# Optimization experiments

Hardware: AMD Instinct MI355X
Metric: run time of the kernel (lower is better)

## Reference

```python
import jax, jax.numpy as jnp
import numpy as np
import math

D_MODEL = 2048
N_HEADS = 16
HEAD_DIM = D_MODEL // N_HEADS  # 128
SEQ = 2048
BATCH = 1


def make_freqs(seq_len, head_dim, theta=10000.0):
    # standard rotary frequencies: freqs_cis = exp(i * t * inv_freq)
    inv_freq = 1.0 / (theta ** (np.arange(0, head_dim, 2, dtype=np.float32) / head_dim))
    t = np.arange(seq_len, dtype=np.float32)
    ang = np.outer(t, inv_freq)  # [seq, head_dim/2]
    return jnp.asarray(np.cos(ang)), jnp.asarray(np.sin(ang))


def setup_inputs() -> dict:
    key = jax.random.key(0)
    ks = jax.random.split(key, 6)
    x = jax.random.normal(ks[0], (BATCH, SEQ, D_MODEL), dtype=jnp.float32)
    freqs_cos, freqs_sin = make_freqs(SEQ, HEAD_DIM)
    # causal additive mask, broadcastable to [b, h, s, s]
    mask = jnp.where(jnp.tril(jnp.ones((SEQ, SEQ), dtype=bool)), 0.0, -1e9).astype(jnp.float32)[None, None]
    scale = 0.02
    wq = jax.random.normal(ks[1], (D_MODEL, D_MODEL), dtype=jnp.float32) * scale
    wk = jax.random.normal(ks[2], (D_MODEL, D_MODEL), dtype=jnp.float32) * scale
    wv = jax.random.normal(ks[3], (D_MODEL, D_MODEL), dtype=jnp.float32) * scale
    wo = jax.random.normal(ks[4], (D_MODEL, D_MODEL), dtype=jnp.float32) * scale
    return {"x": x, "freqs_cos": freqs_cos, "freqs_sin": freqs_sin, "mask": mask,
            "wq": wq, "wk": wk, "wv": wv, "wo": wo}


def _apply_rotary(q, k, cos, sin):
    # q, k: [b, s, h, hd]; cos/sin: [s, hd/2]
    def rot(t):
        tr = t.reshape(*t.shape[:-1], -1, 2)  # [b, s, h, hd/2, 2]
        re, im = tr[..., 0], tr[..., 1]
        c = cos[None, :, None, :]
        s = sin[None, :, None, :]
        # complex multiply (re + i im) * (c + i s)
        out_re = re * c - im * s
        out_im = re * s + im * c
        return jnp.stack([out_re, out_im], axis=-1).reshape(t.shape)
    return rot(q), rot(k)


def reference(x, freqs_cos, freqs_sin, mask, wq, wk, wv, wo):
    b, s, _ = x.shape
    # QKV projections (nn.Linear with no bias: x @ W^T; W is square so use x @ W
    # with W stored already-transposed -- weights here are random so x @ W is faithful math)
    q = (x @ wq).reshape(b, s, N_HEADS, HEAD_DIM)
    k = (x @ wk).reshape(b, s, N_HEADS, HEAD_DIM)
    v = (x @ wv).reshape(b, s, N_HEADS, HEAD_DIM)
    q, k = _apply_rotary(q, k, freqs_cos, freqs_sin)
    # [b, h, s_q, s_k]
    scores = jnp.einsum("bqhd,bkhd->bhqk", q, k) / math.sqrt(HEAD_DIM)
    scores = scores + mask
    probs = jax.nn.softmax(scores.astype(jnp.float32), axis=-1).astype(q.dtype)
    out = jnp.einsum("bhqk,bkhd->bqhd", probs, v).reshape(b, s, N_HEADS * HEAD_DIM)
    return out @ wo
```

## Files before the change

### kernel.cpp

```cpp
#include <hip/hip_runtime.h>
#include <hip/hip_bf16.h>
#include <math.h>

#define SEQ 2048
#define DM 2048
#define NH 16
#define HD 128
#define QKV_N 6144

typedef __bf16 bf16;
typedef __bf16 bf16x8 __attribute__((ext_vector_type(8)));
typedef __bf16 bf16x4v __attribute__((ext_vector_type(4)));
typedef __bf16 bf16x2v __attribute__((ext_vector_type(2)));
typedef float f32x4 __attribute__((ext_vector_type(4)));

__device__ inline int sw_idx64(int row, int chunk) {
    return (row * 8 + (chunk ^ (row & 7))) * 8;
}
__device__ inline int sw_idx128(int row, int chunk) {
    return (row * 16 + (chunk ^ (row & 15))) * 8;
}

__device__ inline void async16(const void* g, void* l) {
    __builtin_amdgcn_global_load_lds((const __attribute__((address_space(1))) void*)g,
                                     (__attribute__((address_space(3))) void*)l, 16, 0, 0);
}

__global__ __launch_bounds__(256) void k_prep(const float* __restrict__ wq,
                                              const float* __restrict__ wk,
                                              const float* __restrict__ wv,
                                              const float* __restrict__ wo,
                                              bf16* __restrict__ wT, bf16* __restrict__ woT,
                                              const float* __restrict__ x,
                                              bf16* __restrict__ xb) {
    const int z = blockIdx.z;
    const int t = threadIdx.x;
    if (z == 4) {
        int bid = blockIdx.y * 32 + blockIdx.x;
#pragma unroll
        for (int j = 0; j < 4; ++j) {
            int i = bid * 1024 + j * 256 + t;
            float4 v = ((const float4*)x)[i];
            bf16x4v o;
            o.x = (bf16)v.x; o.y = (bf16)v.y; o.z = (bf16)v.z; o.w = (bf16)v.w;
            ((bf16x4v*)xb)[i] = o;
        }
        return;
    }
    __shared__ bf16 tile[64][66];
    const float* src = (z == 0) ? wq : (z == 1) ? wk : (z == 2) ? wv : wo;
    bf16* dst = (z < 3) ? (wT + (size_t)z * DM * DM) : woT;
    const int bx = blockIdx.x * 64, by = blockIdx.y * 64;
#pragma unroll
    for (int j = 0; j < 4; ++j) {
        int idx = j * 256 + t;
        int r = idx >> 4, cg = idx & 15;
        float4 v = *(const float4*)&src[(size_t)(by + r) * DM + bx + cg * 4];
        bf16x4v o;
        o.x = (bf16)v.x; o.y = (bf16)v.y; o.z = (bf16)v.z; o.w = (bf16)v.w;
        *(bf16x4v*)&tile[r][cg * 4] = o;
    }
    __syncthreads();
#pragma unroll
    for (int j = 0; j < 4; ++j) {
        int idx = j * 256 + t;
        int r = idx >> 4, cg = idx & 15;
        bf16x4v o;
        o.x = tile[cg * 4 + 0][r];
        o.y = tile[cg * 4 + 1][r];
        o.z = tile[cg * 4 + 2][r];
        o.w = tile[cg * 4 + 3][r];
        *(bf16x4v*)&dst[(size_t)(bx + r) * DM + by + cg * 4] = o;
    }
}

__global__ __launch_bounds__(256) void k_rope_vt(bf16* __restrict__ qkv,
                                                 const float* __restrict__ cosT,
                                                 const float* __restrict__ sinT,
                                                 bf16* __restrict__ vT) {
    const int t = threadIdx.x;
    if (blockIdx.x >= 1024) {
        int g = (blockIdx.x - 1024) * 256 + t;
        int s = g >> 8;
        int cg = g & 255;
        int h = cg >> 4, w8 = cg & 15;
        size_t base = (size_t)s * QKV_N + DM + h * HD + w8 * 8;
        float4 cv = *(const float4*)&cosT[s * 64 + w8 * 4];
        float4 sv = *(const float4*)&sinT[s * 64 + w8 * 4];
        float cc[4] = {cv.x, cv.y, cv.z, cv.w};
        float ss[4] = {sv.x, sv.y, sv.z, sv.w};
        bf16x8 k = *(bf16x8*)&qkv[base];
        bf16x8 o;
#pragma unroll
        for (int p = 0; p < 4; ++p) {
            float re = (float)k[2 * p], im = (float)k[2 * p + 1];
            o[2 * p]     = (bf16)(re * cc[p] - im * ss[p]);
            o[2 * p + 1] = (bf16)(re * ss[p] + im * cc[p]);
        }
        *(bf16x8*)&qkv[base] = o;
        return;
    }
    __shared__ bf16 tile[64][66];
    const int bx = (blockIdx.x & 31) * 64, by = (blockIdx.x >> 5) * 64;
#pragma unroll
    for (int j = 0; j < 4; ++j) {
        int idx = j * 256 + t;
        int r = idx >> 4, cg = idx & 15;
        *(bf16x4v*)&tile[r][cg * 4] =
            *(const bf16x4v*)&qkv[(size_t)(by + r) * QKV_N + 2 * DM + bx + cg * 4];
    }
    __syncthreads();
#pragma unroll
    for (int j = 0; j < 4; ++j) {
        int idx = j * 256 + t;
        int r = idx >> 4, cg = idx & 15;
        bf16x4v o;
        o.x = tile[cg * 4 + 0][r];
        o.y = tile[cg * 4 + 1][r];
        o.z = tile[cg * 4 + 2][r];
        o.w = tile[cg * 4 + 3][r];
        *(bf16x4v*)&vT[(size_t)(bx + r) * SEQ + by + cg * 4] = o;
    }
}

template <typename OutT, int BN>
__device__ __forceinline__ void gemm_body(const bf16* __restrict__ A,
                                          const bf16* __restrict__ Bt,
                                          OutT* __restrict__ C,
                                          int N, int K, size_t bm, size_t bn,
                                          bf16* As, bf16* Bs) {
    constexpr int NI = BN / 32;
    const int t = threadIdx.x;
    const int lane = t & 63;
    const int w = t >> 6;
    const int wr = (w >> 1) * 64, wc = (w & 1) * (BN / 2);
    const int l15 = lane & 15, quad = lane >> 4;
    f32x4 acc[4][NI];
#pragma unroll
    for (int i = 0; i < 4; ++i)
#pragma unroll
        for (int j = 0; j < NI; ++j) acc[i][j] = (f32x4){0.f, 0.f, 0.f, 0.f};

    for (int kt = 0; kt < K; kt += 64) {
#pragma unroll
        for (int j = 0; j < 4; ++j) {
            int c = j * 256 + t;
            int row = c >> 3, g = ((c & 7) ^ (row & 7)) * 8;
            async16(&A[(bm + row) * K + kt + g], &As[c * 8]);
        }
#pragma unroll
        for (int j = 0; j < NI; ++j) {
            int c = j * 256 + t;
            int row = c >> 3, g = ((c & 7) ^ (row & 7)) * 8;
            async16(&Bt[(bn + row) * K + kt + g], &Bs[c * 8]);
        }
        __syncthreads();
#pragma unroll
        for (int kh = 0; kh < 2; ++kh) {
            bf16x8 af[4], bfm[NI];
#pragma unroll
            for (int mi = 0; mi < 4; ++mi)
                af[mi] = *(const bf16x8*)&As[sw_idx64(wr + mi * 16 + l15, kh * 4 + quad)];
#pragma unroll
            for (int ni = 0; ni < NI; ++ni)
                bfm[ni] = *(const bf16x8*)&Bs[sw_idx64(wc + ni * 16 + l15, kh * 4 + quad)];
#pragma unroll
            for (int mi = 0; mi < 4; ++mi)
#pragma unroll
                for (int ni = 0; ni < NI; ++ni)
                    acc[mi][ni] = __builtin_amdgcn_mfma_f32_16x16x32_bf16(
                        af[mi], bfm[ni], acc[mi][ni], 0, 0, 0);
        }
        __syncthreads();
    }
#pragma unroll
    for (int mi = 0; mi < 4; ++mi)
#pragma unroll
        for (int ni = 0; ni < NI; ++ni)
#pragma unroll
            for (int r = 0; r < 4; ++r) {
                size_t row = bm + wr + mi * 16 + quad * 4 + r;
                size_t col = bn + wc + ni * 16 + l15;
                C[row * (size_t)N + col] = (OutT)acc[mi][ni][r];
            }
}

template <typename OutT, int BN>
__global__ __launch_bounds__(256) void k_gemm_bt(const bf16* __restrict__ A,
                                                 const bf16* __restrict__ Bt,
                                                 OutT* __restrict__ C,
                                                 int M, int N, int K) {
    __shared__ bf16 As[128 * 64];
    __shared__ bf16 Bs[BN * 64];
    size_t bm = (size_t)blockIdx.y * 128, bn = (size_t)blockIdx.x * BN;
    gemm_body<OutT, BN>(A, Bt, C, N, K, bm, bn, As, Bs);
}

__global__ __launch_bounds__(256) void k_flash(const bf16* __restrict__ qkv,
                                               const bf16* __restrict__ vT,
                                               const float* __restrict__ cosT,
                                               const float* __restrict__ sinT,
                                               bf16* __restrict__ out) {
    __shared__ bf16 Ks[2][64 * 128];
    __shared__ bf16 Vs[2][128 * 64];
    __shared__ bf16 Pl[4][16 * 64];
    const int t = threadIdx.x;
    const int lane = t & 63;
    const int w = t >> 6;
    const int l15 = lane & 15, quad = lane >> 4;
    const int b = blockIdx.x;
    const int h = (b & 7) * 2 + ((b >> 3) & 1);
    const int qb = (b < 256) ? (31 - (b >> 4)) : ((b >> 4) - 16);
    const int q0w = qb * 64 + w * 16;
    const float sc2 = 0.08838834764831845f * 1.4426950408889634f;

    const size_t qrow = (size_t)(q0w + l15) * QKV_N + h * HD;
    bf16x8 aq[4];
#pragma unroll
    for (int u = 0; u < 4; ++u)
        aq[u] = *(const bf16x8*)&qkv[qrow + u * 32 + quad * 8];
#pragma unroll
    for (int u = 0; u < 4; ++u) {
        float4 cv = *(const float4*)&cosT[(q0w + l15) * 64 + u * 16 + quad * 4];
        float4 sv = *(const float4*)&sinT[(q0w + l15) * 64 + u * 16 + quad * 4];
        float cc[4] = {cv.x, cv.y, cv.z, cv.w};
        float ss[4] = {sv.x, sv.y, sv.z, sv.w};
        bf16x8 q = aq[u], rq;
#pragma unroll
        for (int p = 0; p < 4; ++p) {
            float re = (float)q[2 * p], im = (float)q[2 * p + 1];
            rq[2 * p]     = (bf16)(re * cc[p] - im * ss[p]);
            rq[2 * p + 1] = (bf16)(re * ss[p] + im * cc[p]);
        }
        aq[u] = rq;
    }

    f32x4 o[8];
#pragma unroll
    for (int c = 0; c < 8; ++c) o[c] = (f32x4){0.f, 0.f, 0.f, 0.f};
    float l_r[4] = {0.f, 0.f, 0.f, 0.f};

    int krow[4], kg[4], vrow[4], vg[4];
#pragma unroll
    for (int j = 0; j < 4; ++j) {
        int c = j * 256 + t;
        krow[j] = c >> 4; kg[j] = ((c & 15) ^ (krow[j] & 15)) * 8;
        vrow[j] = c >> 3; vg[j] = ((c & 7) ^ (vrow[j] & 7)) * 8;
    }
    auto stage = [&](int buf, int kt2) {
        const int kb2 = kt2 * 64;
#pragma unroll
        for (int j = 0; j < 4; ++j)
            async16(&qkv[(size_t)(kb2 + krow[j]) * QKV_N + DM + h * HD + kg[j]],
                    &Ks[buf][(j * 256 + t) * 8]);
#pragma unroll
        for (int j = 0; j < 4; ++j)
            async16(&vT[(size_t)(h * HD + vrow[j]) * SEQ + kb2 + vg[j]],
                    &Vs[buf][(j * 256 + t) * 8]);
    };

    const int n64 = qb + 1;
    stage(0, 0);
    for (int kt = 0; kt < n64; ++kt) {
        const int cb = kt & 1;
        const int kbase = kt * 64;
        const bool pre = (kt + 1 < n64);
        if (pre) {
            stage(cb ^ 1, kt + 1);
            asm volatile("s_waitcnt vmcnt(12)" ::: "memory");
        } else {
            asm volatile("s_waitcnt vmcnt(4)" ::: "memory");
        }
        __builtin_amdgcn_s_barrier();
        asm volatile("" ::: "memory");

        f32x4 s4[4];
        __builtin_amdgcn_s_setprio(1);
#pragma unroll
        for (int sub = 0; sub < 4; ++sub) {
            f32x4 z = (f32x4){0.f, 0.f, 0.f, 0.f};
#pragma unroll
            for (int u = 0; u < 4; ++u) {
                bf16x8 kv = *(const bf16x8*)&Ks[cb][sw_idx128(sub * 16 + l15, u * 4 + quad)];
                z = __builtin_amdgcn_mfma_f32_16x16x32_bf16(aq[u], kv, z, 0, 0, 0);
            }
            s4[sub] = z;
        }
        __builtin_amdgcn_s_setprio(0);
        const bool masked = (kt == n64 - 1);
#pragma unroll
        for (int sub = 0; sub < 4; ++sub)
#pragma unroll
            for (int r = 0; r < 4; ++r) {
                float p = __builtin_amdgcn_exp2f(s4[sub][r] * sc2);
                if (masked)
                    p = (kbase + sub * 16 + l15 <= q0w + quad * 4 + r) ? p : 0.f;
                l_r[r] += p;
                int rowp = quad * 4 + r;
                int col = sub * 16 + l15;
                Pl[w][(rowp * 8 + ((col >> 3) ^ (rowp & 7))) * 8 + (col & 7)] = (bf16)p;
            }
        if (pre) asm volatile("s_waitcnt vmcnt(8)" ::: "memory");
        else     asm volatile("s_waitcnt vmcnt(0)" ::: "memory");
        __builtin_amdgcn_s_barrier();
        __asm__ __volatile__("s_waitcnt lgkmcnt(0)" ::: "memory");
        bf16x8 pf[2];
#pragma unroll
        for (int kk = 0; kk < 2; ++kk)
            pf[kk] = *(const bf16x8*)&Pl[w][sw_idx64(l15, kk * 4 + quad)];
        __builtin_amdgcn_s_setprio(1);
#pragma unroll
        for (int c = 0; c < 8; ++c)
#pragma unroll
            for (int kk = 0; kk < 2; ++kk) {
                bf16x8 vb = *(const bf16x8*)&Vs[cb][sw_idx64(c * 16 + l15, kk * 4 + quad)];
                o[c] = __builtin_amdgcn_mfma_f32_16x16x32_bf16(pf[kk], vb, o[c], 0, 0, 0);
            }
        __builtin_amdgcn_s_setprio(0);
        asm volatile("" ::: "memory");
        __builtin_amdgcn_s_barrier();
        asm volatile("" ::: "memory");
    }

    float rl[4];
#pragma unroll
    for (int r = 0; r < 4; ++r) {
        float l = l_r[r];
        l += __shfl_xor(l, 1, 16);
        l += __shfl_xor(l, 2, 16);
        l += __shfl_xor(l, 4, 16);
        l += __shfl_xor(l, 8, 16);
        rl[r] = 1.0f / l;
    }
#pragma unroll
    for (int c = 0; c < 8; ++c)
#pragma unroll
        for (int r = 0; r < 4; ++r)
            out[(size_t)(q0w + quad * 4 + r) * DM + h * HD + c * 16 + l15] =
                (bf16)(o[c][r] * rl[r]);
}

extern "C" void kernel_launch(void* const* d_in, const int* in_sizes, int n_in,
                              void* d_out, int out_size, void* d_ws, size_t ws_size,
                              hipStream_t stream) {
    const float* x  = (const float*)d_in[0];
    const float* fc = (const float*)d_in[1];
    const float* fs = (const float*)d_in[2];
    const float* wq = (const float*)d_in[4];
    const float* wk = (const float*)d_in[5];
    const float* wv = (const float*)d_in[6];
    const float* wo = (const float*)d_in[7];
    float* out = (float*)d_out;

    char* ws = (char*)d_ws;
    bf16* xb  = (bf16*)(ws);
    bf16* wT  = (bf16*)(ws + (size_t)(8u  << 20));
    bf16* woT = (bf16*)(ws + (size_t)(32u << 20));
    bf16* qkv = (bf16*)(ws + (size_t)(40u << 20));
    bf16* vT  = (bf16*)(ws + (size_t)(64u << 20));

    k_prep<<<dim3(32, 32, 5), 256, 0, stream>>>(wq, wk, wv, wo, wT, woT, x, xb);
    k_gemm_bt<bf16, 128><<<dim3(48, 16), 256, 0, stream>>>(xb, wT, qkv, SEQ, QKV_N, DM);
    k_rope_vt<<<3072, 256, 0, stream>>>(qkv, fc, fs, vT);
    k_flash<<<512, 256, 0, stream>>>(qkv, vT, fc, fs, xb);
    k_gemm_bt<float, 64><<<dim3(32, 16), 256, 0, stream>>>(xb, woT, out, SEQ, DM, DM);
}
```

Measured before the change: 285.5 us.

## Pair high and low causal query blocks in one 512-thread flash block sharing K/V

The flash attention kernel now runs 256 blocks of 512 threads. Each block pairs a long causal query block (31-p) with a short one (p) for the same head, and both 4-wave groups share the same staged K/V tiles. This halves global K/V traffic for the short block's tiles and balances work per block. The cost is that the low-block waves sit idle at barriers once they pass their last tile, while the block keeps looping for the high block. Larger blocks may also reduce occupancy.

```diff
diff --git a/kernel.cpp b/kernel.cpp
--- a/kernel.cpp
+++ b/kernel.cpp
@@ -196,22 +196,27 @@
     gemm_body<OutT, BN>(A, Bt, C, N, K, bm, bn, As, Bs);
 }
 
-__global__ __launch_bounds__(256) void k_flash(const bf16* __restrict__ qkv,
+__global__ __launch_bounds__(512) void k_flash(const bf16* __restrict__ qkv,
                                                const bf16* __restrict__ vT,
                                                const float* __restrict__ cosT,
                                                const float* __restrict__ sinT,
                                                bf16* __restrict__ out) {
     __shared__ bf16 Ks[2][64 * 128];
     __shared__ bf16 Vs[2][128 * 64];
-    __shared__ bf16 Pl[4][16 * 64];
+    __shared__ bf16 Pl[8][16 * 64];
     const int t = threadIdx.x;
     const int lane = t & 63;
     const int w = t >> 6;
+    const int wl = w & 3;
+    const int g = w >> 2;
     const int l15 = lane & 15, quad = lane >> 4;
     const int b = blockIdx.x;
-    const int h = (b & 7) * 2 + ((b >> 3) & 1);
-    const int qb = (b < 256) ? (31 - (b >> 4)) : ((b >> 4) - 16);
-    const int q0w = qb * 64 + w * 16;
+    const int hc = b & 15;
+    const int h = (hc & 7) * 2 + (hc >> 3);
+    const int p = b >> 4;
+    const int qbH = 31 - p, qbL = p;
+    const int myQb = g ? qbL : qbH;
+    const int q0w = myQb * 64 + wl * 16;
     const float sc2 = 0.08838834764831845f * 1.4426950408889634f;
 
     const size_t qrow = (size_t)(q0w + l15) * QKV_N + h * HD;
@@ -227,10 +232,10 @@
         float ss[4] = {sv.x, sv.y, sv.z, sv.w};
         bf16x8 q = aq[u], rq;
 #pragma unroll
-        for (int p = 0; p < 4; ++p) {
-            float re = (float)q[2 * p], im = (float)q[2 * p + 1];
-            rq[2 * p]     = (bf16)(re * cc[p] - im * ss[p]);
-            rq[2 * p + 1] = (bf16)(re * ss[p] + im * cc[p]);
+        for (int pp = 0; pp < 4; ++pp) {
+            float re = (float)q[2 * pp], im = (float)q[2 * pp + 1];
+            rq[2 * pp]     = (bf16)(re * cc[pp] - im * ss[pp]);
+            rq[2 * pp + 1] = (bf16)(re * ss[pp] + im * cc[pp]);
         }
         aq[u] = rq;
     }
@@ -240,83 +245,88 @@
     for (int c = 0; c < 8; ++c) o[c] = (f32x4){0.f, 0.f, 0.f, 0.f};
     float l_r[4] = {0.f, 0.f, 0.f, 0.f};
 
-    int krow[4], kg[4], vrow[4], vg[4];
-#pragma unroll
-    for (int j = 0; j < 4; ++j) {
-        int c = j * 256 + t;
-        krow[j] = c >> 4; kg[j] = ((c & 15) ^ (krow[j] & 15)) * 8;
-        vrow[j] = c >> 3; vg[j] = ((c & 7) ^ (vrow[j] & 7)) * 8;
+    int krow[2], kg[2], vrow[2], vg[2];
+#pragma unroll
+    for (int j = 0; j < 2; ++j) {
+        int c2 = j * 512 + t;
+        krow[j] = c2 >> 4; kg[j] = ((c2 & 15) ^ (krow[j] & 15)) * 8;
+        vrow[j] = c2 >> 3; vg[j] = ((c2 & 7) ^ (vrow[j] & 7)) * 8;
     }
     auto stage = [&](int buf, int kt2) {
         const int kb2 = kt2 * 64;
 #pragma unroll
-        for (int j = 0; j < 4; ++j)
+        for (int j = 0; j < 2; ++j)
             async16(&qkv[(size_t)(kb2 + krow[j]) * QKV_N + DM + h * HD + kg[j]],
-                    &Ks[buf][(j * 256 + t) * 8]);
-#pragma unroll
-        for (int j = 0; j < 4; ++j)
+                    &Ks[buf][(j * 512 + t) * 8]);
+#pragma unroll
+        for (int j = 0; j < 2; ++j)
             async16(&vT[(size_t)(h * HD + vrow[j]) * SEQ + kb2 + vg[j]],
-                    &Vs[buf][(j * 256 + t) * 8]);
+                    &Vs[buf][(j * 512 + t) * 8]);
     };
 
-    const int n64 = qb + 1;
+    const int nT = qbH + 1;
     stage(0, 0);
-    for (int kt = 0; kt < n64; ++kt) {
+    for (int kt = 0; kt < nT; ++kt) {
         const int cb = kt & 1;
         const int kbase = kt * 64;
-        const bool pre = (kt + 1 < n64);
+        const bool pre = (kt + 1 < nT);
         if (pre) {
             stage(cb ^ 1, kt + 1);
-            asm volatile("s_waitcnt vmcnt(12)" ::: "memory");
+            asm volatile("s_waitcnt vmcnt(6)" ::: "memory");
         } else {
-            asm volatile("s_waitcnt vmcnt(4)" ::: "memory");
+            asm volatile("s_waitcnt vmcnt(2)" ::: "memory");
         }
         __builtin_amdgcn_s_barrier();
         asm volatile("" ::: "memory");
 
-        f32x4 s4[4];
-        __builtin_amdgcn_s_setprio(1);
-#pragma unroll
-        for (int sub = 0; sub < 4; ++sub) {
-            f32x4 z = (f32x4){0.f, 0.f, 0.f, 0.f};
-#pragma unroll
-            for (int u = 0; u < 4; ++u) {
-                bf16x8 kv = *(const bf16x8*)&Ks[cb][sw_idx128(sub * 16 + l15, u * 4 + quad)];
-                z = __builtin_amdgcn_mfma_f32_16x16x32_bf16(aq[u], kv, z, 0, 0, 0);
+        const bool active = (kt <= myQb);
+        if (active) {
+            f32x4 s4[4];
+            __builtin_amdgcn_s_setprio(1);
+#pragma unroll
+            for (int sub = 0; sub < 4; ++sub) {
+                f32x4 z = (f32x4){0.f, 0.f, 0.f, 0.f};
+#pragma unroll
+                for (int u = 0; u < 4; ++u) {
+                    bf16x8 kv = *(const bf16x8*)&Ks[cb][sw_idx128(sub * 16 + l15, u * 4 + quad)];
+                    z = __builtin_amdgcn_mfma_f32_16x16x32_bf16(aq[u], kv, z, 0, 0, 0);
+                }
+                s4[sub] = z;
             }
-            s4[sub] = z;
-        }
-        __builtin_amdgcn_s_setprio(0);
-        const bool masked = (kt == n64 - 1);
-#pragma unroll
-        for (int sub = 0; sub < 4; ++sub)
-#pragma unroll
-            for (int r = 0; r < 4; ++r) {
-                float p = __builtin_amdgcn_exp2f(s4[sub][r] * sc2);
-                if (masked)
-                    p = (kbase + sub * 16 + l15 <= q0w + quad * 4 + r) ? p : 0.f;
-                l_r[r] += p;
-                int rowp = quad * 4 + r;
-                int col = sub * 16 + l15;
-                Pl[w][(rowp * 8 + ((col >> 3) ^ (rowp & 7))) * 8 + (col & 7)] = (bf16)p;
-            }
-        if (pre) asm volatile("s_waitcnt vmcnt(8)" ::: "memory");
+            __builtin_amdgcn_s_setprio(0);
+            const bool masked = (kt == myQb);
+#pragma unroll
+            for (int sub = 0; sub < 4; ++sub)
+#pragma unroll
+                for (int r = 0; r < 4; ++r) {
+                    float pv = __builtin_amdgcn_exp2f(s4[sub][r] * sc2);
+                    if (masked)
+                        pv = (kbase + sub * 16 + l15 <= q0w + quad * 4 + r) ? pv : 0.f;
+                    l_r[r] += pv;
+                    int rowp = quad * 4 + r;
+                    int col = sub * 16 + l15;
+                    Pl[w][(rowp * 8 + ((col >> 3) ^ (rowp & 7))) * 8 + (col & 7)] = (bf16)pv;
+                }
+        }
+        if (pre) asm volatile("s_waitcnt vmcnt(4)" ::: "memory");
         else     asm volatile("s_waitcnt vmcnt(0)" ::: "memory");
         __builtin_amdgcn_s_barrier();
-        __asm__ __volatile__("s_waitcnt lgkmcnt(0)" ::: "memory");
-        bf16x8 pf[2];
-#pragma unroll
-        for (int kk = 0; kk < 2; ++kk)
-            pf[kk] = *(const bf16x8*)&Pl[w][sw_idx64(l15, kk * 4 + quad)];
-        __builtin_amdgcn_s_setprio(1);
-#pragma unroll
-        for (int c = 0; c < 8; ++c)
-#pragma unroll
-            for (int kk = 0; kk < 2; ++kk) {
-                bf16x8 vb = *(const bf16x8*)&Vs[cb][sw_idx64(c * 16 + l15, kk * 4 + quad)];
-                o[c] = __builtin_amdgcn_mfma_f32_16x16x32_bf16(pf[kk], vb, o[c], 0, 0, 0);
-            }
-        __builtin_amdgcn_s_setprio(0);
+        if (active) {
+            __asm__ __volatile__("s_waitcnt lgkmcnt(0)" ::: "memory");
+            bf16x8 pf[2];
+#pragma unroll
+            for (int kk = 0; kk < 2; ++kk)
+                pf[kk] = *(const bf16x8*)&Pl[w][sw_idx64(l15, kk * 4 + quad)];
+            __builtin_amdgcn_s_setprio(1);
+#pragma unroll
+            for (int c = 0; c < 8; ++c)
+#pragma unroll
+                for (int kk = 0; kk < 2; ++kk) {
+                    bf16x8 vb = *(const bf16x8*)&Vs[cb][sw_idx64(c * 16 + l15, kk * 4 + quad)];
+                    o[c] = __builtin_amdgcn_mfma_f32_16x16x32_bf16(pf[kk], vb, o[c], 0, 0, 0);
+                }
+            __builtin_amdgcn_s_setprio(0);
+        }
         asm volatile("" ::: "memory");
         __builtin_amdgcn_s_barrier();
         asm volatile("" ::: "memory");
@@ -362,6 +372,6 @@
     k_prep<<<dim3(32, 32, 5), 256, 0, stream>>>(wq, wk, wv, wo, wT, woT, x, xb);
     k_gemm_bt<bf16, 128><<<dim3(48, 16), 256, 0, stream>>>(xb, wT, qkv, SEQ, QKV_N, DM);
     k_rope_vt<<<3072, 256, 0, stream>>>(qkv, fc, fs, vT);
-    k_flash<<<512, 256, 0, stream>>>(qkv, vT, fc, fs, xb);
+    k_flash<<<256, 512, 0, stream>>>(qkv, vT, fc, fs, xb);
     k_gemm_bt<float, 64><<<dim3(32, 16), 256, 0, stream>>>(xb, woT, out, SEQ, DM, DM);
 }
```

Result: no change. 290.8 us (+1.9%).

## Split flash attention over key ranges with 128-row query tiles and combine pass

Applied to the files above, without the earlier changes.

The flash kernel now processes 128 query rows per block, 32 per wave in two 16-row groups, so each K/V tile loaded to LDS feeds twice as many MFMAs. Each query tile's key range is split into two segments handled by separate blocks, giving every block the same number of key tiles (qt+1), which balances causal work. The blocks write unnormalized fp32 partial outputs and row sums, and a new k_ocomb kernel adds them, normalizes and writes bf16. In exchange it adds fp32 partial-output traffic and an extra launch, applies the causal mask compare on every tile, and uses more registers per wave.

```diff
diff --git a/kernel.cpp b/kernel.cpp
--- a/kernel.cpp
+++ b/kernel.cpp
@@ -200,45 +200,57 @@
                                                const bf16* __restrict__ vT,
                                                const float* __restrict__ cosT,
                                                const float* __restrict__ sinT,
-                                               bf16* __restrict__ out) {
+                                               float* __restrict__ oP0,
+                                               float* __restrict__ oP1,
+                                               float* __restrict__ lP) {
     __shared__ bf16 Ks[2][64 * 128];
     __shared__ bf16 Vs[2][128 * 64];
-    __shared__ bf16 Pl[4][16 * 64];
+    __shared__ bf16 Pl[4][32 * 64];
     const int t = threadIdx.x;
     const int lane = t & 63;
     const int w = t >> 6;
     const int l15 = lane & 15, quad = lane >> 4;
     const int b = blockIdx.x;
-    const int h = (b & 7) * 2 + ((b >> 3) & 1);
-    const int qb = (b < 256) ? (31 - (b >> 4)) : ((b >> 4) - 16);
-    const int q0w = qb * 64 + w * 16;
+    const int hc = b & 15;
+    const int h = (hc & 7) * 2 + (hc >> 3);
+    const int u = (b >> 4) & 15;
+    const int seg = b >> 8;
+    const int qt = seg ? u : 15 - u;
+    const int q0w = qt * 128 + w * 32;
+    const int kt0 = seg ? (qt + 1) : 0;
+    const int nT = qt + 1;
     const float sc2 = 0.08838834764831845f * 1.4426950408889634f;
-
-    const size_t qrow = (size_t)(q0w + l15) * QKV_N + h * HD;
-    bf16x8 aq[4];
-#pragma unroll
-    for (int u = 0; u < 4; ++u)
-        aq[u] = *(const bf16x8*)&qkv[qrow + u * 32 + quad * 8];
-#pragma unroll
-    for (int u = 0; u < 4; ++u) {
-        float4 cv = *(const float4*)&cosT[(q0w + l15) * 64 + u * 16 + quad * 4];
-        float4 sv = *(const float4*)&sinT[(q0w + l15) * 64 + u * 16 + quad * 4];
-        float cc[4] = {cv.x, cv.y, cv.z, cv.w};
-        float ss[4] = {sv.x, sv.y, sv.z, sv.w};
-        bf16x8 q = aq[u], rq;
-#pragma unroll
-        for (int p = 0; p < 4; ++p) {
-            float re = (float)q[2 * p], im = (float)q[2 * p + 1];
-            rq[2 * p]     = (bf16)(re * cc[p] - im * ss[p]);
-            rq[2 * p + 1] = (bf16)(re * ss[p] + im * cc[p]);
-        }
-        aq[u] = rq;
-    }
-
-    f32x4 o[8];
-#pragma unroll
-    for (int c = 0; c < 8; ++c) o[c] = (f32x4){0.f, 0.f, 0.f, 0.f};
-    float l_r[4] = {0.f, 0.f, 0.f, 0.f};
+    float* oSeg = seg ? oP1 : oP0;
+
+    bf16x8 aq[2][4];
+#pragma unroll
+    for (int rg = 0; rg < 2; ++rg) {
+        const int qrow = q0w + rg * 16 + l15;
+        const size_t qbase = (size_t)qrow * QKV_N + h * HD;
+#pragma unroll
+        for (int u4 = 0; u4 < 4; ++u4) {
+            bf16x8 q = *(const bf16x8*)&qkv[qbase + u4 * 32 + quad * 8];
+            float4 cv = *(const float4*)&cosT[qrow * 64 + u4 * 16 + quad * 4];
+            float4 sv = *(const float4*)&sinT[qrow * 64 + u4 * 16 + quad * 4];
+            float cc[4] = {cv.x, cv.y, cv.z, cv.w};
+            float ss[4] = {sv.x, sv.y, sv.z, sv.w};
+            bf16x8 rq;
+#pragma unroll
+            for (int pp = 0; pp < 4; ++pp) {
+                float re = (float)q[2 * pp], im = (float)q[2 * pp + 1];
+                rq[2 * pp]     = (bf16)(re * cc[pp] - im * ss[pp]);
+                rq[2 * pp + 1] = (bf16)(re * ss[pp] + im * cc[pp]);
+            }
+            aq[rg][u4] = rq;
+        }
+    }
+
+    f32x4 o[2][8];
+#pragma unroll
+    for (int rg = 0; rg < 2; ++rg)
+#pragma unroll
+        for (int c = 0; c < 8; ++c) o[rg][c] = (f32x4){0.f, 0.f, 0.f, 0.f};
+    float l_r[2][4] = {{0.f, 0.f, 0.f, 0.f}, {0.f, 0.f, 0.f, 0.f}};
 
     int krow[4], kg[4], vrow[4], vg[4];
 #pragma unroll
@@ -259,12 +271,12 @@
                     &Vs[buf][(j * 256 + t) * 8]);
     };
 
-    const int n64 = qb + 1;
-    stage(0, 0);
-    for (int kt = 0; kt < n64; ++kt) {
-        const int cb = kt & 1;
+    stage(0, kt0);
+    for (int i = 0; i < nT; ++i) {
+        const int kt = kt0 + i;
+        const int cb = i & 1;
         const int kbase = kt * 64;
-        const bool pre = (kt + 1 < n64);
+        const bool pre = (i + 1 < nT);
         if (pre) {
             stage(cb ^ 1, kt + 1);
             asm volatile("s_waitcnt vmcnt(12)" ::: "memory");
@@ -274,47 +286,55 @@
         __builtin_amdgcn_s_barrier();
         asm volatile("" ::: "memory");
 
-        f32x4 s4[4];
+        f32x4 s4[2][4];
         __builtin_amdgcn_s_setprio(1);
 #pragma unroll
         for (int sub = 0; sub < 4; ++sub) {
-            f32x4 z = (f32x4){0.f, 0.f, 0.f, 0.f};
-#pragma unroll
-            for (int u = 0; u < 4; ++u) {
-                bf16x8 kv = *(const bf16x8*)&Ks[cb][sw_idx128(sub * 16 + l15, u * 4 + quad)];
-                z = __builtin_amdgcn_mfma_f32_16x16x32_bf16(aq[u], kv, z, 0, 0, 0);
+            f32x4 z0 = (f32x4){0.f, 0.f, 0.f, 0.f};
+            f32x4 z1 = (f32x4){0.f, 0.f, 0.f, 0.f};
+#pragma unroll
+            for (int u4 = 0; u4 < 4; ++u4) {
+                bf16x8 kv = *(const bf16x8*)&Ks[cb][sw_idx128(sub * 16 + l15, u4 * 4 + quad)];
+                z0 = __builtin_amdgcn_mfma_f32_16x16x32_bf16(aq[0][u4], kv, z0, 0, 0, 0);
+                z1 = __builtin_amdgcn_mfma_f32_16x16x32_bf16(aq[1][u4], kv, z1, 0, 0, 0);
             }
-            s4[sub] = z;
+            s4[0][sub] = z0;
+            s4[1][sub] = z1;
         }
         __builtin_amdgcn_s_setprio(0);
-        const bool masked = (kt == n64 - 1);
-#pragma unroll
-        for (int sub = 0; sub < 4; ++sub)
-#pragma unroll
-            for (int r = 0; r < 4; ++r) {
-                float p = __builtin_amdgcn_exp2f(s4[sub][r] * sc2);
-                if (masked)
-                    p = (kbase + sub * 16 + l15 <= q0w + quad * 4 + r) ? p : 0.f;
-                l_r[r] += p;
-                int rowp = quad * 4 + r;
-                int col = sub * 16 + l15;
-                Pl[w][(rowp * 8 + ((col >> 3) ^ (rowp & 7))) * 8 + (col & 7)] = (bf16)p;
-            }
+#pragma unroll
+        for (int rg = 0; rg < 2; ++rg)
+#pragma unroll
+            for (int sub = 0; sub < 4; ++sub)
+#pragma unroll
+                for (int r = 0; r < 4; ++r) {
+                    float pv = __builtin_amdgcn_exp2f(s4[rg][sub][r] * sc2);
+                    int key = kbase + sub * 16 + l15;
+                    int row = q0w + rg * 16 + quad * 4 + r;
+                    pv = (key <= row) ? pv : 0.f;
+                    l_r[rg][r] += pv;
+                    int rp = rg * 16 + quad * 4 + r;
+                    int col = sub * 16 + l15;
+                    Pl[w][sw_idx64(rp, col >> 3) + (col & 7)] = (bf16)pv;
+                }
         if (pre) asm volatile("s_waitcnt vmcnt(8)" ::: "memory");
         else     asm volatile("s_waitcnt vmcnt(0)" ::: "memory");
         __builtin_amdgcn_s_barrier();
         __asm__ __volatile__("s_waitcnt lgkmcnt(0)" ::: "memory");
-        bf16x8 pf[2];
-#pragma unroll
-        for (int kk = 0; kk < 2; ++kk)
-            pf[kk] = *(const bf16x8*)&Pl[w][sw_idx64(l15, kk * 4 + quad)];
+        bf16x8 pf[2][2];
+#pragma unroll
+        for (int rg = 0; rg < 2; ++rg)
+#pragma unroll
+            for (int kk = 0; kk < 2; ++kk)
+                pf[rg][kk] = *(const bf16x8*)&Pl[w][sw_idx64(rg * 16 + l15, kk * 4 + quad)];
         __builtin_amdgcn_s_setprio(1);
 #pragma unroll
         for (int c = 0; c < 8; ++c)
 #pragma unroll
             for (int kk = 0; kk < 2; ++kk) {
                 bf16x8 vb = *(const bf16x8*)&Vs[cb][sw_idx64(c * 16 + l15, kk * 4 + quad)];
-                o[c] = __builtin_amdgcn_mfma_f32_16x16x32_bf16(pf[kk], vb, o[c], 0, 0, 0);
+                o[0][c] = __builtin_amdgcn_mfma_f32_16x16x32_bf16(pf[0][kk], vb, o[0][c], 0, 0, 0);
+                o[1][c] = __builtin_amdgcn_mfma_f32_16x16x32_bf16(pf[1][kk], vb, o[1][c], 0, 0, 0);
             }
         __builtin_amdgcn_s_setprio(0);
         asm volatile("" ::: "memory");
@@ -322,22 +342,44 @@
         asm volatile("" ::: "memory");
     }
 
-    float rl[4];
-#pragma unroll
-    for (int r = 0; r < 4; ++r) {
-        float l = l_r[r];
-        l += __shfl_xor(l, 1, 16);
-        l += __shfl_xor(l, 2, 16);
-        l += __shfl_xor(l, 4, 16);
-        l += __shfl_xor(l, 8, 16);
-        rl[r] = 1.0f / l;
-    }
-#pragma unroll
-    for (int c = 0; c < 8; ++c)
-#pragma unroll
-        for (int r = 0; r < 4; ++r)
-            out[(size_t)(q0w + quad * 4 + r) * DM + h * HD + c * 16 + l15] =
-                (bf16)(o[c][r] * rl[r]);
+#pragma unroll
+    for (int rg = 0; rg < 2; ++rg)
+#pragma unroll
+        for (int r = 0; r < 4; ++r) {
+            float l = l_r[rg][r];
+            l += __shfl_xor(l, 1, 16);
+            l += __shfl_xor(l, 2, 16);
+            l += __shfl_xor(l, 4, 16);
+            l += __shfl_xor(l, 8, 16);
+            int row = q0w + rg * 16 + quad * 4 + r;
+            if (l15 == 0) lP[seg * 32768 + row * 16 + h] = l;
+#pragma unroll
+            for (int c = 0; c < 8; ++c)
+                oSeg[(size_t)row * DM + h * HD + c * 16 + l15] = o[rg][c][r];
+        }
+}
+
+__global__ __launch_bounds__(256) void k_ocomb(const float* __restrict__ oP0,
+                                               const float* __restrict__ oP1,
+                                               const float* __restrict__ lP,
+                                               bf16* __restrict__ xb) {
+    int idx = blockIdx.x * 256 + threadIdx.x;
+    int row = idx >> 8;
+    int cg = idx & 255;
+    int h = cg >> 4, c8 = cg & 15;
+    size_t base = (size_t)row * DM + h * HD + c8 * 8;
+    f32x4 a0 = *(const f32x4*)&oP0[base];
+    f32x4 a1 = *(const f32x4*)&oP0[base + 4];
+    f32x4 b0 = *(const f32x4*)&oP1[base];
+    f32x4 b1 = *(const f32x4*)&oP1[base + 4];
+    float rl = 1.0f / (lP[row * 16 + h] + lP[32768 + row * 16 + h]);
+    bf16x8 o8;
+#pragma unroll
+    for (int j = 0; j < 4; ++j) {
+        o8[j]     = (bf16)((a0[j] + b0[j]) * rl);
+        o8[4 + j] = (bf16)((a1[j] + b1[j]) * rl);
+    }
+    *(bf16x8*)&xb[base] = o8;
 }
 
 extern "C" void kernel_launch(void* const* d_in, const int* in_sizes, int n_in,
@@ -353,15 +395,19 @@
     float* out = (float*)d_out;
 
     char* ws = (char*)d_ws;
-    bf16* xb  = (bf16*)(ws);
-    bf16* wT  = (bf16*)(ws + (size_t)(8u  << 20));
-    bf16* woT = (bf16*)(ws + (size_t)(32u << 20));
-    bf16* qkv = (bf16*)(ws + (size_t)(40u << 20));
-    bf16* vT  = (bf16*)(ws + (size_t)(64u << 20));
+    bf16*  xb  = (bf16*)(ws);
+    bf16*  wT  = (bf16*)(ws + (size_t)(8u  << 20));
+    float* oP0 = (float*)(ws + (size_t)(8u  << 20));
+    bf16*  woT = (bf16*)(ws + (size_t)(32u << 20));
+    bf16*  qkv = (bf16*)(ws + (size_t)(40u << 20));
+    bf16*  vT  = (bf16*)(ws + (size_t)(64u << 20));
+    float* oP1 = (float*)(ws + (size_t)(72u << 20));
+    float* lP  = (float*)(ws + (size_t)(88u << 20));
 
     k_prep<<<dim3(32, 32, 5), 256, 0, stream>>>(wq, wk, wv, wo, wT, woT, x, xb);
     k_gemm_bt<bf16, 128><<<dim3(48, 16), 256, 0, stream>>>(xb, wT, qkv, SEQ, QKV_N, DM);
     k_rope_vt<<<3072, 256, 0, stream>>>(qkv, fc, fs, vT);
-    k_flash<<<512, 256, 0, stream>>>(qkv, vT, fc, fs, xb);
+    k_flash<<<512, 256, 0, stream>>>(qkv, vT, fc, fs, oP0, oP1, lP);
+    k_ocomb<<<2048, 256, 0, stream>>>(oP0, oP1, lP, xb);
     k_gemm_bt<float, 64><<<dim3(32, 16), 256, 0, stream>>>(xb, woT, out, SEQ, DM, DM);
 }
```

New measurement: 285.3 us. No clear change (-0.1%).
